# Kernel tuning notes

Measured on AMD Instinct MI355X. Metric: run time of the kernel, lower is better.

The kernel has to match this reference:

```python
import jax, jax.numpy as jnp
import numpy as np

HIDDEN = 2048
HEADS = 16
HEAD_DIM = HIDDEN // HEADS


def setup_inputs() -> dict:
    key = jax.random.key(0)
    ks = jax.random.split(key, 9)
    s = 1.0 / np.sqrt(HIDDEN)
    return {
        "hidden_states": jax.random.normal(ks[0], (2, 2048, HIDDEN), dtype=jnp.float32),
        "wq": jax.random.uniform(ks[1], (HIDDEN, HIDDEN), jnp.float32, -s, s),
        "bq": jax.random.uniform(ks[2], (HIDDEN,), jnp.float32, -s, s),
        "wk": jax.random.uniform(ks[3], (HIDDEN, HIDDEN), jnp.float32, -s, s),
        "bk": jax.random.uniform(ks[4], (HIDDEN,), jnp.float32, -s, s),
        "wv": jax.random.uniform(ks[5], (HIDDEN, HIDDEN), jnp.float32, -s, s),
        "bv": jax.random.uniform(ks[6], (HIDDEN,), jnp.float32, -s, s),
        "wo": jax.random.uniform(ks[7], (HIDDEN, HIDDEN), jnp.float32, -s, s),
        "bo": jax.random.uniform(ks[8], (HIDDEN,), jnp.float32, -s, s),
    }


def reference(hidden_states, wq, bq, wk, bk, wv, bv, wo, bo):
    B, S, _ = hidden_states.shape
    # QKV projections (nn.Linear: x @ W^T + b)
    q = hidden_states @ wq.T + bq
    k = hidden_states @ wk.T + bk
    v = hidden_states @ wv.T + bv
    # [B, S, H, D] -> [B, H, S, D]
    q = q.reshape(B, S, HEADS, HEAD_DIM).transpose(0, 2, 1, 3)
    k = k.reshape(B, S, HEADS, HEAD_DIM).transpose(0, 2, 1, 3)
    v = v.reshape(B, S, HEADS, HEAD_DIM).transpose(0, 2, 1, 3)
    scale = HEAD_DIM ** (-0.5)
    scores = jnp.einsum("bhqd,bhkd->bhqk", q, k) * scale  # [B,H,S,S]
    attn = jax.nn.softmax(scores, axis=-1)
    out = jnp.einsum("bhqk,bhkd->bhqd", attn, v)
    out = out.transpose(0, 2, 1, 3).reshape(B, S, HIDDEN)
    return out @ wo.T + bo
```

## Files before the change

kernel.cpp:

```cpp
#include <hip/hip_runtime.h>
#include <math.h>

#define HID 2048
#define NB  2
#define SEQ 2048
#define NT  (NB*SEQ)
#define NH  16
#define HD  128

typedef __attribute__((ext_vector_type(8))) _Float16       f16x8;
typedef __attribute__((ext_vector_type(2))) __fp16         h16x2;
typedef __attribute__((ext_vector_type(4))) float          f32x4;

#define QSCALE 0.12751742f

__device__ __forceinline__ unsigned short f2h(float x) {
    union { _Float16 h; unsigned short u; } c;
    c.h = (_Float16)x;
    return c.u;
}

extern "C" __global__ __launch_bounds__(256)
void cast_all(const float* __restrict__ X,
              const float* __restrict__ w0, const float* __restrict__ w1,
              const float* __restrict__ w2, const float* __restrict__ w3,
              unsigned short* __restrict__ Xd,
              unsigned short* __restrict__ d0, unsigned short* __restrict__ d1,
              unsigned short* __restrict__ d2, unsigned short* __restrict__ d3,
              int n4x, int n4w)
{
    const int y = blockIdx.y;
    const float* __restrict__ src =
        (y==0) ? X : (y==1) ? w0 : (y==2) ? w1 : (y==3) ? w2 : w3;
    unsigned short* __restrict__ dst =
        (y==0) ? Xd : (y==1) ? d0 : (y==2) ? d1 : (y==3) ? d2 : d3;
    const int n4 = (y==0) ? n4x : n4w;
    const int i = blockIdx.x * 256 + threadIdx.x;
    if (i >= n4) return;
    const float4 x = ((const float4*)src)[i];
    ushort4 h;
    h.x = f2h(x.x); h.y = f2h(x.y); h.z = f2h(x.z); h.w = f2h(x.w);
    ((ushort4*)dst)[i] = h;
}

extern "C" __global__ __launch_bounds__(256)
void qkv_f16(const unsigned short* __restrict__ Xh,
             const unsigned short* __restrict__ Wqh,
             const unsigned short* __restrict__ Wkh,
             const unsigned short* __restrict__ Wvh,
             const float* __restrict__ bq, const float* __restrict__ bk,
             const float* __restrict__ bv,
             unsigned short* __restrict__ Qb, unsigned short* __restrict__ Kb,
             unsigned short* __restrict__ Vb)
{
    const int on0 = blockIdx.x * 128;
    const int tm0 = blockIdx.y * 128;
    const int which = blockIdx.z;
    const unsigned short* __restrict__ W = (which==0) ? Wqh : (which==1) ? Wkh : Wvh;
    const float* __restrict__ bias      = (which==0) ? bq  : (which==1) ? bk  : bv;

    __shared__ unsigned short Ah[8192], Bh[8192];

    const int tid  = threadIdx.x;
    const int lane = tid & 63;
    const int w    = tid >> 6;
    const int wm   = (w & 1) * 64;
    const int wn   = (w >> 1) * 64;
    const int fr   = lane & 15;
    const int quad = lane >> 4;

    f32x4 acc[4][4];
    #pragma unroll
    for (int i = 0; i < 4; ++i)
        #pragma unroll
        for (int j = 0; j < 4; ++j)
            acc[i][j] = (f32x4){0.f, 0.f, 0.f, 0.f};

    for (int kb = 0; kb < HID/64; ++kb) {
        __syncthreads();
        const unsigned short* Asrc = Xh + (size_t)tm0*HID + kb*64;
        const unsigned short* Bsrc = W  + (size_t)on0*HID + kb*64;
        #pragma unroll
        for (int r = 0; r < 4; ++r) {
            const int p   = (r*4 + w)*64 + lane;
            const int row = p >> 3;
            const int c   = (p & 7) ^ (row & 7);
            __builtin_amdgcn_global_load_lds(
                (const __attribute__((address_space(1))) void*)(Asrc + (size_t)row*HID + c*8),
                (__attribute__((address_space(3))) void*)(Ah + (r*4 + w)*512), 16, 0, 0);
            __builtin_amdgcn_global_load_lds(
                (const __attribute__((address_space(1))) void*)(Bsrc + (size_t)row*HID + c*8),
                (__attribute__((address_space(3))) void*)(Bh + (r*4 + w)*512), 16, 0, 0);
        }
        __syncthreads();

        #pragma unroll
        for (int kk = 0; kk < 2; ++kk) {
            f16x8 a[4], b[4];
            #pragma unroll
            for (int i = 0; i < 4; ++i) {
                const int ra = wm + i*16 + fr;
                a[i] = *(const f16x8*)(Ah + (ra*8 + ((kk*4 + quad) ^ (ra & 7)))*8);
                const int rb = wn + i*16 + fr;
                b[i] = *(const f16x8*)(Bh + (rb*8 + ((kk*4 + quad) ^ (rb & 7)))*8);
            }
            #pragma unroll
            for (int i = 0; i < 4; ++i)
                #pragma unroll
                for (int j = 0; j < 4; ++j)
                    acc[i][j] = __builtin_amdgcn_mfma_f32_16x16x32_f16(a[i], b[j], acc[i][j], 0, 0, 0);
        }
    }

    const int col_l = fr;
    if (which == 2) {
        #pragma unroll
        for (int j = 0; j < 4; ++j) {
            const int o = on0 + wn + j*16 + col_l;
            const float bb = bias[o];
            const int h = o >> 7, d = o & (HD-1);
            #pragma unroll
            for (int i = 0; i < 4; ++i)
                #pragma unroll
                for (int rg = 0; rg < 4; ++rg) {
                    const int t = tm0 + wm + i*16 + quad*4 + rg;
                    const int b = t >> 11, s = t & (SEQ-1);
                    const int pos = (s & ~63) | (((s & 15) << 2) | ((s >> 4) & 3));
                    Vb[((size_t)(b*NH + h)*HD + d)*SEQ + pos] = f2h(acc[i][j][rg] + bb);
                }
        }
    } else {
        const float sc = (which == 0) ? QSCALE : 1.0f;
        unsigned short* __restrict__ dstp = (which == 0) ? Qb : Kb;
        #pragma unroll
        for (int j = 0; j < 4; ++j) {
            const int o = on0 + wn + j*16 + col_l;
            const float bb = bias[o];
            const int h = o >> 7, d = o & (HD-1);
            #pragma unroll
            for (int i = 0; i < 4; ++i)
                #pragma unroll
                for (int rg = 0; rg < 4; ++rg) {
                    const int t = tm0 + wm + i*16 + quad*4 + rg;
                    const int b = t >> 11, s = t & (SEQ-1);
                    dstp[((size_t)(b*NH + h)*SEQ + s)*HD + d] =
                        f2h((acc[i][j][rg] + bb) * sc);
                }
        }
    }
}

#define PS_STRIDE 72

extern "C" __global__ __launch_bounds__(512, 4)
void attn_mfma(const unsigned short* __restrict__ Qg, const unsigned short* __restrict__ Kg,
               const unsigned short* __restrict__ Vtg, unsigned short* __restrict__ Of)
{
    const int L  = blockIdx.x;
    const int q0 = (L >> 5) * 128;
    const int bh = ((L & 7) << 2) | ((L >> 3) & 3);
    const unsigned short* __restrict__ Qp = Qg  + (size_t)bh * SEQ * HD;
    const unsigned short* __restrict__ Kp = Kg  + (size_t)bh * SEQ * HD;
    const unsigned short* __restrict__ Vp = Vtg + (size_t)bh * HD * SEQ;

    __shared__ alignas(16) unsigned short Ks[64*128];
    __shared__ alignas(16) unsigned short Vts[128*64];
    __shared__ alignas(16) unsigned short Ps[8][16*PS_STRIDE];

    const int tid  = threadIdx.x;
    const int lane = tid & 63;
    const int w    = tid >> 6;
    const int fr   = lane & 15;
    const int quad = lane >> 4;

    f16x8 qf[4];
    #pragma unroll
    for (int c = 0; c < 4; ++c)
        qf[c] = *(const f16x8*)(Qp + (size_t)(q0 + w*16 + fr)*HD + c*32 + quad*8);

    f32x4 accO[8];
    #pragma unroll
    for (int n = 0; n < 8; ++n)
        accO[n] = (f32x4){0.f, 0.f, 0.f, 0.f};
    float lp[4] = {};

    for (int kt = 0; kt < SEQ/64; ++kt) {
        __syncthreads();
        {
            const unsigned short* Kt = Kp + (size_t)kt*64*HD;
            #pragma unroll
            for (int r = 0; r < 2; ++r) {
                const int p   = (r*8 + w)*64 + lane;
                const int row = p >> 4;
                const int c   = (p & 15) ^ (row & 15);
                __builtin_amdgcn_global_load_lds(
                    (const __attribute__((address_space(1))) void*)(Kt + (size_t)row*HD + c*8),
                    (__attribute__((address_space(3))) void*)(Ks + (r*8 + w)*512), 16, 0, 0);
            }
            #pragma unroll
            for (int r = 0; r < 2; ++r) {
                const int p   = (r*8 + w)*64 + lane;
                const int row = p >> 3;
                const int c   = (p & 7) ^ (row & 7);
                __builtin_amdgcn_global_load_lds(
                    (const __attribute__((address_space(1))) void*)(Vp + (size_t)row*SEQ + kt*64 + c*8),
                    (__attribute__((address_space(3))) void*)(Vts + (r*8 + w)*512), 16, 0, 0);
            }
        }
        __syncthreads();

        f32x4 accS[4];
        #pragma unroll
        for (int n = 0; n < 4; ++n)
            accS[n] = (f32x4){0.f, 0.f, 0.f, 0.f};
        #pragma unroll
        for (int c = 0; c < 4; ++c) {
            f16x8 bf[4];
            #pragma unroll
            for (int n = 0; n < 4; ++n)
                bf[n] = *(const f16x8*)(Ks + (n*16 + fr)*128 + ((c*4 + quad) ^ fr)*8);
            __builtin_amdgcn_s_setprio(1);
            #pragma unroll
            for (int n = 0; n < 4; ++n)
                accS[n] = __builtin_amdgcn_mfma_f32_16x16x32_f16(
                    qf[c], bf[n], accS[n], 0, 0, 0);
            __builtin_amdgcn_s_setprio(0);
        }

        #pragma unroll
        for (int rg = 0; rg < 4; ++rg) {
            float p0 = exp2f(accS[0][rg]);
            float p1 = exp2f(accS[1][rg]);
            float p2 = exp2f(accS[2][rg]);
            float p3 = exp2f(accS[3][rg]);
            lp[rg] += (p0 + p1) + (p2 + p3);
            union { h16x2 h[2]; ushort4 u4; } pk;
            pk.h[0] = __builtin_amdgcn_cvt_pkrtz(p0, p1);
            pk.h[1] = __builtin_amdgcn_cvt_pkrtz(p2, p3);
            *(ushort4*)(&Ps[w][(quad*4 + rg)*PS_STRIDE + fr*4]) = pk.u4;
        }

        #pragma unroll
        for (int cc = 0; cc < 2; ++cc) {
            f16x8 pf = *(const f16x8*)(&Ps[w][fr*PS_STRIDE + cc*32 + quad*8]);
            f16x8 vf[8];
            #pragma unroll
            for (int n = 0; n < 8; ++n)
                vf[n] = *(const f16x8*)(Vts + (n*16 + fr)*64 + ((cc*4 + quad) ^ (fr & 7))*8);
            __builtin_amdgcn_s_setprio(1);
            #pragma unroll
            for (int n = 0; n < 8; ++n)
                accO[n] = __builtin_amdgcn_mfma_f32_16x16x32_f16(
                    pf, vf[n], accO[n], 0, 0, 0);
            __builtin_amdgcn_s_setprio(0);
        }
    }

    float inv[4];
    #pragma unroll
    for (int rg = 0; rg < 4; ++rg) {
        float l = lp[rg];
        l += __shfl_xor(l, 1);
        l += __shfl_xor(l, 2);
        l += __shfl_xor(l, 4);
        l += __shfl_xor(l, 8);
        inv[rg] = 1.0f / l;
    }
    const int bb_ = bh >> 4;
    const int hh_ = bh & (NH - 1);
    #pragma unroll
    for (int n = 0; n < 8; ++n) {
        const int d = n*16 + fr;
        #pragma unroll
        for (int rg = 0; rg < 4; ++rg) {
            const int s = q0 + w*16 + quad*4 + rg;
            Of[((size_t)(bb_*SEQ + s))*HID + hh_*HD + d] = f2h(accO[n][rg] * inv[rg]);
        }
    }
}

extern "C" __global__ __launch_bounds__(256)
void oproj_f16(const unsigned short* __restrict__ Af,
               const unsigned short* __restrict__ Woh,
               const float* __restrict__ bo, float* __restrict__ Y)
{
    const int on0 = blockIdx.x * 128;
    const int tm0 = blockIdx.y * 64;

    __shared__ unsigned short Ah[4096], Bh[8192];

    const int tid  = threadIdx.x;
    const int lane = tid & 63;
    const int w    = tid >> 6;
    const int wm   = (w & 1) * 32;
    const int wn   = (w >> 1) * 64;
    const int fr   = lane & 15;
    const int quad = lane >> 4;

    f32x4 acc[2][4];
    #pragma unroll
    for (int i = 0; i < 2; ++i)
        #pragma unroll
        for (int j = 0; j < 4; ++j)
            acc[i][j] = (f32x4){0.f, 0.f, 0.f, 0.f};

    for (int kb = 0; kb < HID/64; ++kb) {
        __syncthreads();
        const unsigned short* Asrc = Af  + (size_t)tm0*HID + kb*64;
        const unsigned short* Bsrc = Woh + (size_t)on0*HID + kb*64;
        #pragma unroll
        for (int r = 0; r < 2; ++r) {
            const int p   = r*256 + tid;
            const int row = p >> 3;
            const int c   = (p & 7) ^ (row & 7);
            __builtin_amdgcn_global_load_lds(
                (const __attribute__((address_space(1))) void*)(Asrc + (size_t)row*HID + c*8),
                (__attribute__((address_space(3))) void*)(Ah + p*8), 16, 0, 0);
        }
        #pragma unroll
        for (int r = 0; r < 4; ++r) {
            const int p   = r*256 + tid;
            const int row = p >> 3;
            const int c   = (p & 7) ^ (row & 7);
            __builtin_amdgcn_global_load_lds(
                (const __attribute__((address_space(1))) void*)(Bsrc + (size_t)row*HID + c*8),
                (__attribute__((address_space(3))) void*)(Bh + p*8), 16, 0, 0);
        }
        __syncthreads();

        #pragma unroll
        for (int kk = 0; kk < 2; ++kk) {
            f16x8 a[2], b[4];
            #pragma unroll
            for (int i = 0; i < 2; ++i) {
                const int ra = wm + i*16 + fr;
                a[i] = *(const f16x8*)(Ah + (ra*8 + ((kk*4 + quad) ^ (ra & 7)))*8);
            }
            #pragma unroll
            for (int j = 0; j < 4; ++j) {
                const int rb = wn + j*16 + fr;
                b[j] = *(const f16x8*)(Bh + (rb*8 + ((kk*4 + quad) ^ (rb & 7)))*8);
            }
            #pragma unroll
            for (int i = 0; i < 2; ++i)
                #pragma unroll
                for (int j = 0; j < 4; ++j)
                    acc[i][j] = __builtin_amdgcn_mfma_f32_16x16x32_f16(a[i], b[j], acc[i][j], 0, 0, 0);
        }
    }

    #pragma unroll
    for (int j = 0; j < 4; ++j) {
        const int o = on0 + wn + j*16 + fr;
        const float bb = bo[o];
        #pragma unroll
        for (int i = 0; i < 2; ++i)
            #pragma unroll
            for (int rg = 0; rg < 4; ++rg) {
                const int t = tm0 + wm + i*16 + quad*4 + rg;
                Y[(size_t)t*HID + o] = acc[i][j][rg] + bb;
            }
    }
}

extern "C" void kernel_launch(void* const* d_in, const int* in_sizes, int n_in,
                              void* d_out, int out_size, void* d_ws, size_t ws_size,
                              hipStream_t stream)
{
    const float* X  = (const float*)d_in[0];
    const float* wq = (const float*)d_in[1];
    const float* bq = (const float*)d_in[2];
    const float* wk = (const float*)d_in[3];
    const float* bk = (const float*)d_in[4];
    const float* wv = (const float*)d_in[5];
    const float* bv = (const float*)d_in[6];
    const float* wo = (const float*)d_in[7];
    const float* bo = (const float*)d_in[8];
    float* Y = (float*)d_out;

    const size_t F  = (size_t)NT * HID;
    const size_t Wn = (size_t)HID * HID;

    unsigned short* Qb  = (unsigned short*)d_ws;
    unsigned short* Kb  = Qb  + F;
    unsigned short* Vb  = Kb  + F;
    unsigned short* Of  = Vb  + F;
    unsigned short* Xh  = Of  + F;
    unsigned short* Wqh = Xh  + F;
    unsigned short* Wkh = Wqh + Wn;
    unsigned short* Wvh = Wkh + Wn;
    unsigned short* Woh = Wvh + Wn;

    const int n4x = (int)(F/4);
    const int n4w = (int)(Wn/4);

    cast_all<<<dim3((n4x + 255)/256, 5), 256, 0, stream>>>(
        X, wq, wk, wv, wo, Xh, Wqh, Wkh, Wvh, Woh, n4x, n4w);

    qkv_f16<<<dim3(HID/128, NT/128, 3), 256, 0, stream>>>(
        Xh, Wqh, Wkh, Wvh, bq, bk, bv, Qb, Kb, Vb);

    attn_mfma<<<dim3(512, 1, 1), 512, 0, stream>>>(Qb, Kb, Vb, Of);

    oproj_f16<<<dim3(HID/128, NT/64), 256, 0, stream>>>(Of, Woh, bo, Y);
}
```

Measured before the change: 396.5 us.

## Double-buffer K/V tiles and split attention work into 2x2 warp tiles with shared P

```diff
diff --git a/kernel.cpp b/kernel.cpp
--- a/kernel.cpp
+++ b/kernel.cpp
@@ -9,7 +9,6 @@
 #define HD  128
 
 typedef __attribute__((ext_vector_type(8))) _Float16       f16x8;
-typedef __attribute__((ext_vector_type(2))) __fp16         h16x2;
 typedef __attribute__((ext_vector_type(4))) float          f32x4;
 
 #define QSCALE 0.12751742f
@@ -125,8 +124,7 @@
                 for (int rg = 0; rg < 4; ++rg) {
                     const int t = tm0 + wm + i*16 + quad*4 + rg;
                     const int b = t >> 11, s = t & (SEQ-1);
-                    const int pos = (s & ~63) | (((s & 15) << 2) | ((s >> 4) & 3));
-                    Vb[((size_t)(b*NH + h)*HD + d)*SEQ + pos] = f2h(acc[i][j][rg] + bb);
+                    Vb[((size_t)(b*NH + h)*HD + d)*SEQ + s] = f2h(acc[i][j][rg] + bb);
                 }
         }
     } else {
@@ -149,8 +147,6 @@
         }
     }
 }
-
-#define PS_STRIDE 72
 
 extern "C" __global__ __launch_bounds__(512, 4)
 void attn_mfma(const unsigned short* __restrict__ Qg, const unsigned short* __restrict__ Kg,
@@ -163,118 +159,170 @@
     const unsigned short* __restrict__ Kp = Kg  + (size_t)bh * SEQ * HD;
     const unsigned short* __restrict__ Vp = Vtg + (size_t)bh * HD * SEQ;
 
-    __shared__ alignas(16) unsigned short Ks[64*128];
-    __shared__ alignas(16) unsigned short Vts[128*64];
-    __shared__ alignas(16) unsigned short Ps[8][16*PS_STRIDE];
+    __shared__ alignas(16) unsigned short Ks[2][64*128];
+    __shared__ alignas(16) unsigned short Vts[2][128*64];
+    __shared__ alignas(16) unsigned short Ps[128*64];
 
     const int tid  = threadIdx.x;
     const int lane = tid & 63;
     const int w    = tid >> 6;
+    const int iq   = w >> 1;
+    const int js   = w & 1;
     const int fr   = lane & 15;
     const int quad = lane >> 4;
 
-    f16x8 qf[4];
-    #pragma unroll
-    for (int c = 0; c < 4; ++c)
-        qf[c] = *(const f16x8*)(Qp + (size_t)(q0 + w*16 + fr)*HD + c*32 + quad*8);
-
-    f32x4 accO[8];
-    #pragma unroll
-    for (int n = 0; n < 8; ++n)
-        accO[n] = (f32x4){0.f, 0.f, 0.f, 0.f};
-    float lp[4] = {};
-
+    f16x8 qf[2][4];
+    #pragma unroll
+    for (int m = 0; m < 2; ++m)
+        #pragma unroll
+        for (int c = 0; c < 4; ++c)
+            qf[m][c] = *(const f16x8*)(Qp + (size_t)(q0 + iq*32 + m*16 + fr)*HD
+                                          + c*32 + quad*8);
+
+    f32x4 accO[2][4];
+    #pragma unroll
+    for (int m = 0; m < 2; ++m)
+        #pragma unroll
+        for (int n = 0; n < 4; ++n)
+            accO[m][n] = (f32x4){0.f, 0.f, 0.f, 0.f};
+    float lp[2][4] = {};
+
+#define STAGE(buf, kt_) do {                                                   \
+    const unsigned short* _Kt = Kp + (size_t)(kt_)*64*HD;                      \
+    _Pragma("unroll")                                                          \
+    for (int _r = 0; _r < 2; ++_r) {                                           \
+        const int _p = (_r*8 + w)*64 + lane;                                   \
+        const int _row = _p >> 4;                                              \
+        const int _c = (_p & 15) ^ (_row & 15);                                \
+        __builtin_amdgcn_global_load_lds(                                      \
+            (const __attribute__((address_space(1))) void*)(_Kt + (size_t)_row*HD + _c*8), \
+            (__attribute__((address_space(3))) void*)(&Ks[buf][_p*8]), 16, 0, 0); \
+    }                                                                          \
+    _Pragma("unroll")                                                          \
+    for (int _r = 0; _r < 2; ++_r) {                                           \
+        const int _p = (_r*8 + w)*64 + lane;                                   \
+        const int _row = _p >> 3;                                              \
+        const int _c = (_p & 7) ^ (_row & 7);                                  \
+        __builtin_amdgcn_global_load_lds(                                      \
+            (const __attribute__((address_space(1))) void*)(Vp + (size_t)_row*SEQ + (kt_)*64 + _c*8), \
+            (__attribute__((address_space(3))) void*)(&Vts[buf][_p*8]), 16, 0, 0); \
+    } } while (0)
+
+    STAGE(0, 0);
+    __syncthreads();
+
+    int cur = 0;
     for (int kt = 0; kt < SEQ/64; ++kt) {
-        __syncthreads();
-        {
-            const unsigned short* Kt = Kp + (size_t)kt*64*HD;
-            #pragma unroll
-            for (int r = 0; r < 2; ++r) {
-                const int p   = (r*8 + w)*64 + lane;
-                const int row = p >> 4;
-                const int c   = (p & 15) ^ (row & 15);
-                __builtin_amdgcn_global_load_lds(
-                    (const __attribute__((address_space(1))) void*)(Kt + (size_t)row*HD + c*8),
-                    (__attribute__((address_space(3))) void*)(Ks + (r*8 + w)*512), 16, 0, 0);
-            }
-            #pragma unroll
-            for (int r = 0; r < 2; ++r) {
-                const int p   = (r*8 + w)*64 + lane;
-                const int row = p >> 3;
-                const int c   = (p & 7) ^ (row & 7);
-                __builtin_amdgcn_global_load_lds(
-                    (const __attribute__((address_space(1))) void*)(Vp + (size_t)row*SEQ + kt*64 + c*8),
-                    (__attribute__((address_space(3))) void*)(Vts + (r*8 + w)*512), 16, 0, 0);
-            }
-        }
-        __syncthreads();
-
-        f32x4 accS[4];
-        #pragma unroll
-        for (int n = 0; n < 4; ++n)
-            accS[n] = (f32x4){0.f, 0.f, 0.f, 0.f};
+        if (kt + 1 < SEQ/64) STAGE(cur ^ 1, kt + 1);
+
+        const unsigned short* Kc = &Ks[cur][0];
+        const unsigned short* Vc = &Vts[cur][0];
+
+        f32x4 accS[2][2];
+        #pragma unroll
+        for (int m = 0; m < 2; ++m)
+            #pragma unroll
+            for (int n = 0; n < 2; ++n)
+                accS[m][n] = (f32x4){0.f, 0.f, 0.f, 0.f};
         #pragma unroll
         for (int c = 0; c < 4; ++c) {
-            f16x8 bf[4];
+            f16x8 bf[2];
+            #pragma unroll
+            for (int n = 0; n < 2; ++n)
+                bf[n] = *(const f16x8*)(Kc + (js*32 + n*16 + fr)*128
+                                           + (((c*4 + quad) ^ fr) << 3));
+            __builtin_amdgcn_s_setprio(1);
+            #pragma unroll
+            for (int m = 0; m < 2; ++m)
+                #pragma unroll
+                for (int n = 0; n < 2; ++n)
+                    accS[m][n] = __builtin_amdgcn_mfma_f32_16x16x32_f16(
+                        qf[m][c], bf[n], accS[m][n], 0, 0, 0);
+            __builtin_amdgcn_s_setprio(0);
+        }
+
+        #pragma unroll
+        for (int m = 0; m < 2; ++m)
+            #pragma unroll
+            for (int n = 0; n < 2; ++n)
+                #pragma unroll
+                for (int rg = 0; rg < 4; ++rg) {
+                    const float p = exp2f(accS[m][n][rg]);
+                    lp[m][rg] += p;
+                    const int q = iq*32 + m*16 + quad*4 + rg;
+                    const int s = js*32 + n*16 + fr;
+                    Ps[q*64 + ((((s >> 3) ^ (q & 7)) << 3) | (s & 7))] = f2h(p);
+                }
+        asm volatile("s_waitcnt lgkmcnt(0)" ::: "memory");
+        __builtin_amdgcn_s_barrier();
+        __builtin_amdgcn_sched_barrier(0);
+
+        #pragma unroll
+        for (int kk = 0; kk < 2; ++kk) {
+            f16x8 pf[2], vf[4];
+            #pragma unroll
+            for (int m = 0; m < 2; ++m)
+                pf[m] = *(const f16x8*)(Ps + (iq*32 + m*16 + fr)*64
+                                           + (((kk*4 + quad) ^ (fr & 7)) << 3));
             #pragma unroll
             for (int n = 0; n < 4; ++n)
-                bf[n] = *(const f16x8*)(Ks + (n*16 + fr)*128 + ((c*4 + quad) ^ fr)*8);
+                vf[n] = *(const f16x8*)(Vc + (js*64 + n*16 + fr)*64
+                                           + (((kk*4 + quad) ^ (fr & 7)) << 3));
             __builtin_amdgcn_s_setprio(1);
             #pragma unroll
-            for (int n = 0; n < 4; ++n)
-                accS[n] = __builtin_amdgcn_mfma_f32_16x16x32_f16(
-                    qf[c], bf[n], accS[n], 0, 0, 0);
+            for (int m = 0; m < 2; ++m)
+                #pragma unroll
+                for (int n = 0; n < 4; ++n)
+                    accO[m][n] = __builtin_amdgcn_mfma_f32_16x16x32_f16(
+                        pf[m], vf[n], accO[m][n], 0, 0, 0);
             __builtin_amdgcn_s_setprio(0);
         }
 
+        asm volatile("s_waitcnt vmcnt(0) lgkmcnt(0)" ::: "memory");
+        __builtin_amdgcn_s_barrier();
+        __builtin_amdgcn_sched_barrier(0);
+        cur ^= 1;
+    }
+#undef STAGE
+
+    float lred[2][4];
+    #pragma unroll
+    for (int m = 0; m < 2; ++m)
         #pragma unroll
         for (int rg = 0; rg < 4; ++rg) {
-            float p0 = exp2f(accS[0][rg]);
-            float p1 = exp2f(accS[1][rg]);
-            float p2 = exp2f(accS[2][rg]);
-            float p3 = exp2f(accS[3][rg]);
-            lp[rg] += (p0 + p1) + (p2 + p3);
-            union { h16x2 h[2]; ushort4 u4; } pk;
-            pk.h[0] = __builtin_amdgcn_cvt_pkrtz(p0, p1);
-            pk.h[1] = __builtin_amdgcn_cvt_pkrtz(p2, p3);
-            *(ushort4*)(&Ps[w][(quad*4 + rg)*PS_STRIDE + fr*4]) = pk.u4;
-        }
-
-        #pragma unroll
-        for (int cc = 0; cc < 2; ++cc) {
-            f16x8 pf = *(const f16x8*)(&Ps[w][fr*PS_STRIDE + cc*32 + quad*8]);
-            f16x8 vf[8];
-            #pragma unroll
-            for (int n = 0; n < 8; ++n)
-                vf[n] = *(const f16x8*)(Vts + (n*16 + fr)*64 + ((cc*4 + quad) ^ (fr & 7))*8);
-            __builtin_amdgcn_s_setprio(1);
-            #pragma unroll
-            for (int n = 0; n < 8; ++n)
-                accO[n] = __builtin_amdgcn_mfma_f32_16x16x32_f16(
-                    pf, vf[n], accO[n], 0, 0, 0);
-            __builtin_amdgcn_s_setprio(0);
-        }
-    }
-
-    float inv[4];
-    #pragma unroll
-    for (int rg = 0; rg < 4; ++rg) {
-        float l = lp[rg];
-        l += __shfl_xor(l, 1);
-        l += __shfl_xor(l, 2);
-        l += __shfl_xor(l, 4);
-        l += __shfl_xor(l, 8);
-        inv[rg] = 1.0f / l;
-    }
+            float l = lp[m][rg];
+            l += __shfl_xor(l, 1);
+            l += __shfl_xor(l, 2);
+            l += __shfl_xor(l, 4);
+            l += __shfl_xor(l, 8);
+            lred[m][rg] = l;
+        }
+    float* Ls = (float*)(&Ks[0][0]);
+    if (fr == 0) {
+        #pragma unroll
+        for (int m = 0; m < 2; ++m)
+            #pragma unroll
+            for (int rg = 0; rg < 4; ++rg)
+                Ls[w*32 + m*16 + quad*4 + rg] = lred[m][rg];
+    }
+    __syncthreads();
+
     const int bb_ = bh >> 4;
     const int hh_ = bh & (NH - 1);
     #pragma unroll
-    for (int n = 0; n < 8; ++n) {
-        const int d = n*16 + fr;
-        #pragma unroll
-        for (int rg = 0; rg < 4; ++rg) {
-            const int s = q0 + w*16 + quad*4 + rg;
-            Of[((size_t)(bb_*SEQ + s))*HID + hh_*HD + d] = f2h(accO[n][rg] * inv[rg]);
+    for (int m = 0; m < 2; ++m) {
+        float inv[4];
+        #pragma unroll
+        for (int rg = 0; rg < 4; ++rg)
+            inv[rg] = 1.0f / (lred[m][rg] + Ls[(w ^ 1)*32 + m*16 + quad*4 + rg]);
+        #pragma unroll
+        for (int n = 0; n < 4; ++n) {
+            const int d = js*64 + n*16 + fr;
+            #pragma unroll
+            for (int rg = 0; rg < 4; ++rg) {
+                const int s = q0 + iq*32 + m*16 + quad*4 + rg;
+                Of[((size_t)(bb_*SEQ + s))*HID + hh_*HD + d] = f2h(accO[m][n][rg] * inv[rg]);
+            }
         }
     }
 }
```

New measurement: 452.6 us. 14.1% more time.
